# Performance work log

Hardware: AMD Instinct MI355X
Metric: run time of the kernel (lower is better)

## Reference

```python
import jax, jax.numpy as jnp
import numpy as np

B, S, E = 2, 2048, 2048
H, HKV, D = 32, 8, 64  # n_heads, n_kv_heads, head_dim


def _rope(x, cos, sin):
    # x: [B,S,h,D]; cos/sin: [1,S,1,D//2]. Complex rotate on (even,odd) pairs.
    xp = x.reshape(*x.shape[:-1], D // 2, 2)
    x0, x1 = xp[..., 0], xp[..., 1]
    r0 = x0 * cos - x1 * sin
    r1 = x0 * sin + x1 * cos
    return jnp.stack([r0, r1], axis=-1).reshape(x.shape)


def setup_inputs() -> dict:
    key = jax.random.key(0)
    ks = jax.random.split(key, 8)
    sc = 0.02
    # real RoPE frequencies (theta=10000) for realism
    inv = 1.0 / (10000.0 ** (np.arange(0, D, 2, dtype=np.float32) / D))
    t = np.arange(S, dtype=np.float32)
    ang = np.outer(t, inv)  # [S, D/2]
    return {
        "x": jax.random.normal(ks[0], (B, S, E), jnp.float32),
        "start_pos": 0,
        "freqs_cos": jnp.asarray(np.cos(ang))[None, :, None, :],
        "freqs_sin": jnp.asarray(np.sin(ang))[None, :, None, :],
        "wq": jax.random.normal(ks[1], (E, H * D), jnp.float32) * sc,
        "wk": jax.random.normal(ks[2], (E, HKV * D), jnp.float32) * sc,
        "wv": jax.random.normal(ks[3], (E, HKV * D), jnp.float32) * sc,
        "out_w": jax.random.normal(ks[4], (H * D, E), jnp.float32) * sc,
        "out_b": jnp.zeros((E,), jnp.float32),
        "k_cache": jnp.zeros((B, S, HKV, D), jnp.float32),
        "v_cache": jnp.zeros((B, S, HKV, D), jnp.float32),
    }


def reference(x, start_pos, freqs_cos, freqs_sin, wq, wk, wv, out_w, out_b, k_cache, v_cache):
    b, s, _ = x.shape
    q = (x @ wq).reshape(b, s, H, D)
    k = (x @ wk).reshape(b, s, HKV, D)
    v = (x @ wv).reshape(b, s, HKV, D)
    q = _rope(q, freqs_cos[:, :s], freqs_sin[:, :s])
    k = _rope(k, freqs_cos[:, :s], freqs_sin[:, :s])
    # KV-cache append (torch code detaches before writing)
    k_cache = jax.lax.dynamic_update_slice(k_cache, jax.lax.stop_gradient(k), (0, start_pos, 0, 0))
    v_cache = jax.lax.dynamic_update_slice(v_cache, jax.lax.stop_gradient(v), (0, start_pos, 0, 0))
    keys = k_cache[:b, : start_pos + s]    # [b, T, HKV, D]
    values = v_cache[:b, : start_pos + s]
    g = H // HKV
    if g > 1:  # GQA head repeat
        keys = jnp.repeat(keys, g, axis=2)     # [b, T, H, D]
        values = jnp.repeat(values, g, axis=2)
    scores = jnp.einsum("bqhd,bkhd->bhqk", q, keys) / jnp.sqrt(jnp.float32(D))
    att = jax.nn.softmax(scores, axis=-1)  # NOTE: source applies no causal mask
    o = jnp.einsum("bhqk,bkhd->bqhd", att, values).reshape(b, s, H * D)
    return o @ out_w + out_b
```

## Files before the change

### kernel.cpp

```cpp
#include <hip/hip_runtime.h>
#include <math.h>

#define B_    2
#define S_    2048
#define E_    2048
#define H_    32
#define HKV_  8
#define D_    64

typedef __bf16 bf16x8 __attribute__((ext_vector_type(8)));
typedef __bf16 bf16x4 __attribute__((ext_vector_type(4)));
typedef float  f32x4  __attribute__((ext_vector_type(4)));

#define GPTR(x) ((const __attribute__((address_space(1))) void*)(x))
#define LPTR(x) ((__attribute__((address_space(3))) void*)(x))

__global__ __launch_bounds__(256) void convert_kernel(
    const float* __restrict__ in, __bf16* __restrict__ out, int n8)
{
    const int i = blockIdx.x * 256 + threadIdx.x;
    if (i >= n8) return;
    const float4 a = ((const float4*)in)[i * 2];
    const float4 b = ((const float4*)in)[i * 2 + 1];
    bf16x8 o;
    o[0] = (__bf16)a.x; o[1] = (__bf16)a.y; o[2] = (__bf16)a.z; o[3] = (__bf16)a.w;
    o[4] = (__bf16)b.x; o[5] = (__bf16)b.y; o[6] = (__bf16)b.z; o[7] = (__bf16)b.w;
    ((bf16x8*)out)[i] = o;
}

__global__ __launch_bounds__(256) void transpose_convert_kernel(
    const float* __restrict__ in, __bf16* __restrict__ out, int K, int N)
{
    __shared__ float tile[32][33];
    const int k0 = blockIdx.y * 32, n0 = blockIdx.x * 32;
    const int r  = threadIdx.x >> 3;
    const int c4 = (threadIdx.x & 7) * 4;
    const float4 v = *(const float4*)&in[(size_t)(k0 + r) * N + n0 + c4];
    tile[r][c4 + 0] = v.x; tile[r][c4 + 1] = v.y;
    tile[r][c4 + 2] = v.z; tile[r][c4 + 3] = v.w;
    __syncthreads();
    ushort4 o;
    __bf16 h0 = (__bf16)tile[c4 + 0][r]; o.x = __builtin_bit_cast(unsigned short, h0);
    __bf16 h1 = (__bf16)tile[c4 + 1][r]; o.y = __builtin_bit_cast(unsigned short, h1);
    __bf16 h2 = (__bf16)tile[c4 + 2][r]; o.z = __builtin_bit_cast(unsigned short, h2);
    __bf16 h3 = (__bf16)tile[c4 + 3][r]; o.w = __builtin_bit_cast(unsigned short, h3);
    *(ushort4*)&out[(size_t)(n0 + r) * K + k0 + c4] = o;
}

__device__ __forceinline__ void gemm_mfma_body(
    const __bf16* __restrict__ A, const __bf16* __restrict__ Bt,
    int m0, int n0, int K, __bf16* sA, __bf16* sB, f32x4 acc[4][4])
{
    const int t    = threadIdx.x;
    const int w    = t >> 6;
    const int lane = t & 63;
    const int col  = lane & 15;
    const int quad = lane >> 4;
    const int wrow = (w >> 1) * 64;
    const int wcol = (w & 1) * 64;

    const int row0 = t >> 3;
    const int c0   = t & 7;

    for (int k0 = 0; k0 < K; k0 += 64) {
#pragma unroll
        for (int it = 0; it < 4; ++it) {
            const int row  = it * 32 + row0;
            const int csrc = c0 ^ (row & 7);
            __builtin_amdgcn_global_load_lds(
                GPTR(A + (size_t)(m0 + row) * K + k0 + csrc * 8),
                LPTR(sA + (it * 256 + t) * 8), 16, 0, 0);
        }
#pragma unroll
        for (int it = 0; it < 4; ++it) {
            const int row  = it * 32 + row0;
            const int csrc = c0 ^ (row & 7);
            __builtin_amdgcn_global_load_lds(
                GPTR(Bt + (size_t)(n0 + row) * K + k0 + csrc * 8),
                LPTR(sB + (it * 256 + t) * 8), 16, 0, 0);
        }
        __syncthreads();

#pragma unroll
        for (int kk = 0; kk < 2; ++kk) {
            bf16x8 af[4], bfr[4];
#pragma unroll
            for (int i = 0; i < 4; ++i) {
                const int m = wrow + i * 16 + col;
                af[i] = *(const bf16x8*)&sA[m * 64 + (((kk * 4 + quad) ^ (m & 7)) * 8)];
            }
#pragma unroll
            for (int j = 0; j < 4; ++j) {
                const int n = wcol + j * 16 + col;
                bfr[j] = *(const bf16x8*)&sB[n * 64 + (((kk * 4 + quad) ^ (n & 7)) * 8)];
            }
#pragma unroll
            for (int i = 0; i < 4; ++i)
#pragma unroll
                for (int j = 0; j < 4; ++j)
                    acc[i][j] = __builtin_amdgcn_mfma_f32_16x16x32_bf16(
                        af[i], bfr[j], acc[i][j], 0, 0, 0);
        }
        __syncthreads();
    }
}

__global__ __launch_bounds__(256) void gemm_qkv_kernel(
    const __bf16* __restrict__ xb, const __bf16* __restrict__ wT,
    __bf16* __restrict__ qb, __bf16* __restrict__ kb, __bf16* __restrict__ vb)
{
    __shared__ __bf16 sA[128 * 64];
    __shared__ __bf16 sB[128 * 64];
    f32x4 acc[4][4];
#pragma unroll
    for (int i = 0; i < 4; ++i)
#pragma unroll
        for (int j = 0; j < 4; ++j) acc[i][j] = (f32x4){0.f, 0.f, 0.f, 0.f};

    const int bx = blockIdx.x;
    const int m0 = blockIdx.y * 128;
    gemm_mfma_body(xb, wT, m0, bx * 128, E_, sA, sB, acc);

    __bf16* Cp; int ldc, nb;
    if (bx < 16)      { Cp = qb; ldc = H_ * D_;   nb = bx * 128; }
    else if (bx < 20) { Cp = kb; ldc = HKV_ * D_; nb = (bx - 16) * 128; }
    else              { Cp = vb; ldc = HKV_ * D_; nb = (bx - 20) * 128; }

    const int lane = threadIdx.x & 63;
    const int col  = lane & 15;
    const int quad = lane >> 4;
    const int wrow = ((threadIdx.x >> 6) >> 1) * 64;
    const int wcol = ((threadIdx.x >> 6) & 1) * 64;
#pragma unroll
    for (int i = 0; i < 4; ++i)
#pragma unroll
        for (int j = 0; j < 4; ++j)
#pragma unroll
            for (int r = 0; r < 4; ++r) {
                const int m = m0 + wrow + i * 16 + quad * 4 + r;
                const int n = nb + wcol + j * 16 + col;
                Cp[(size_t)m * ldc + n] = (__bf16)acc[i][j][r];
            }
}

__global__ __launch_bounds__(256) void gemm_out_kernel(
    const __bf16* __restrict__ ob, const __bf16* __restrict__ woT,
    const float* __restrict__ bias, float* __restrict__ out)
{
    __shared__ __bf16 sA[128 * 64];
    __shared__ __bf16 sB[128 * 64];
    f32x4 acc[4][4];
#pragma unroll
    for (int i = 0; i < 4; ++i)
#pragma unroll
        for (int j = 0; j < 4; ++j) acc[i][j] = (f32x4){0.f, 0.f, 0.f, 0.f};

    const int m0 = blockIdx.y * 128;
    const int n0 = blockIdx.x * 128;
    gemm_mfma_body(ob, woT, m0, n0, H_ * D_, sA, sB, acc);

    const int lane = threadIdx.x & 63;
    const int col  = lane & 15;
    const int quad = lane >> 4;
    const int wrow = ((threadIdx.x >> 6) >> 1) * 64;
    const int wcol = ((threadIdx.x >> 6) & 1) * 64;
#pragma unroll
    for (int i = 0; i < 4; ++i)
#pragma unroll
        for (int j = 0; j < 4; ++j)
#pragma unroll
            for (int r = 0; r < 4; ++r) {
                const int m = m0 + wrow + i * 16 + quad * 4 + r;
                const int n = n0 + wcol + j * 16 + col;
                out[(size_t)m * E_ + n] = acc[i][j][r] + bias[n];
            }
}

__global__ __launch_bounds__(256) void rope_kernel(
    __bf16* __restrict__ p, const float* __restrict__ fc,
    const float* __restrict__ fs, int nh, int npairs)
{
    const int i = blockIdx.x * 256 + threadIdx.x;
    if (i >= npairs) return;
    const int pair = i & 31;
    const int row  = i >> 5;
    const int s    = (row / nh) % S_;
    const unsigned int v = ((const unsigned int*)p)[i];
    const float x0 = (float)__builtin_bit_cast(__bf16, (unsigned short)(v & 0xffff));
    const float x1 = (float)__builtin_bit_cast(__bf16, (unsigned short)(v >> 16));
    const float c  = fc[s * 32 + pair];
    const float sn = fs[s * 32 + pair];
    const __bf16 r0 = (__bf16)(x0 * c - x1 * sn);
    const __bf16 r1 = (__bf16)(x0 * sn + x1 * c);
    ((unsigned int*)p)[i] =
        ((unsigned int)__builtin_bit_cast(unsigned short, r1) << 16) |
        (unsigned int)__builtin_bit_cast(unsigned short, r0);
}

__global__ __launch_bounds__(256, 2) void attn_kernel(
    const __bf16* __restrict__ qw, const __bf16* __restrict__ kw,
    const __bf16* __restrict__ vw, __bf16* __restrict__ ow)
{
    __shared__ __bf16 sK [64][72];
    __shared__ __bf16 sVT[64][72];
    __shared__ __bf16 sP [4][64][72];

    const int t    = threadIdx.x;
    const int w    = t >> 6;
    const int lane = t & 63;
    const int col  = lane & 15;
    const int quad = lane >> 4;

    const int bh  = blockIdx.y;
    const int b   = bh >> 5;
    const int h   = bh & 31;
    const int kvh = h >> 2;
    const int q0w = blockIdx.x * 256 + w * 64;

    const int KSTR = HKV_ * D_;

    bf16x8 bQ[4][2];
#pragma unroll
    for (int qf = 0; qf < 4; ++qf) {
        const __bf16* qrow = qw + (((size_t)b * S_ + q0w + qf * 16 + col) * H_ + h) * D_;
        bQ[qf][0] = ((const bf16x8*)qrow)[quad];
        bQ[qf][1] = ((const bf16x8*)qrow)[4 + quad];
    }

    f32x4 O[4][4];
#pragma unroll
    for (int qf = 0; qf < 4; ++qf)
#pragma unroll
        for (int dt = 0; dt < 4; ++dt) O[qf][dt] = (f32x4){0.f, 0.f, 0.f, 0.f};
    float lr[4] = {0.f, 0.f, 0.f, 0.f};

    const __bf16* kbase = kw + ((size_t)b * S_ * HKV_ + kvh) * D_;
    const __bf16* vbase = vw + ((size_t)b * S_ * HKV_ + kvh) * D_;

    const int kkey = t >> 2;
    const int kd   = (t & 3) * 16;
    const int vkp  = (t & 31) * 2;
    const int vdg  = (t >> 5) * 4;

    for (int j0 = 0; j0 < S_; j0 += 64) {
        {
            const __bf16* kr = kbase + (size_t)(j0 + kkey) * KSTR + kd;
            *(bf16x8*)&sK[kkey][kd]     = ((const bf16x8*)kr)[0];
            *(bf16x8*)&sK[kkey][kd + 8] = ((const bf16x8*)kr)[1];
        }
#pragma unroll
        for (int r = 0; r < 64; r += 32) {
            const __bf16* v0 = vbase + (size_t)(j0 + vkp) * KSTR + vdg + r;
            const __bf16* v1 = v0 + KSTR;
            const ushort4 ua = *(const ushort4*)v0;
            const ushort4 uc = *(const ushort4*)v1;
            *(unsigned int*)&sVT[vdg + r + 0][vkp] = ((unsigned int)uc.x << 16) | ua.x;
            *(unsigned int*)&sVT[vdg + r + 1][vkp] = ((unsigned int)uc.y << 16) | ua.y;
            *(unsigned int*)&sVT[vdg + r + 2][vkp] = ((unsigned int)uc.z << 16) | ua.z;
            *(unsigned int*)&sVT[vdg + r + 3][vkp] = ((unsigned int)uc.w << 16) | ua.w;
        }
        __syncthreads();

#pragma unroll
        for (int st = 0; st < 4; ++st) {
            const bf16x8 aK0 = *(const bf16x8*)&sK[st * 16 + col][quad * 8];
            const bf16x8 aK1 = *(const bf16x8*)&sK[st * 16 + col][32 + quad * 8];
#pragma unroll
            for (int qf = 0; qf < 4; ++qf) {
                f32x4 sc = (f32x4){0.f, 0.f, 0.f, 0.f};
                sc = __builtin_amdgcn_mfma_f32_16x16x32_bf16(aK0, bQ[qf][0], sc, 0, 0, 0);
                sc = __builtin_amdgcn_mfma_f32_16x16x32_bf16(aK1, bQ[qf][1], sc, 0, 0, 0);
                bf16x4 pk;
                float psum = 0.f;
#pragma unroll
                for (int r = 0; r < 4; ++r) {
                    const float p = __expf(sc[r] * 0.125f);
                    psum += p;
                    pk[r] = (__bf16)p;
                }
                lr[qf] += psum;
                *(bf16x4*)&sP[w][qf * 16 + col][st * 16 + quad * 4] = pk;
            }
        }

        bf16x8 vbf[4][2];
#pragma unroll
        for (int dt = 0; dt < 4; ++dt) {
            vbf[dt][0] = *(const bf16x8*)&sVT[dt * 16 + col][quad * 8];
            vbf[dt][1] = *(const bf16x8*)&sVT[dt * 16 + col][32 + quad * 8];
        }
#pragma unroll
        for (int qf = 0; qf < 4; ++qf) {
            const bf16x8 pa0 = *(const bf16x8*)&sP[w][qf * 16 + col][quad * 8];
            const bf16x8 pa1 = *(const bf16x8*)&sP[w][qf * 16 + col][32 + quad * 8];
#pragma unroll
            for (int dt = 0; dt < 4; ++dt) {
                O[qf][dt] = __builtin_amdgcn_mfma_f32_16x16x32_bf16(pa0, vbf[dt][0], O[qf][dt], 0, 0, 0);
                O[qf][dt] = __builtin_amdgcn_mfma_f32_16x16x32_bf16(pa1, vbf[dt][1], O[qf][dt], 0, 0, 0);
            }
        }
        __syncthreads();
    }

#pragma unroll
    for (int qf = 0; qf < 4; ++qf) {
        lr[qf] += __shfl_xor(lr[qf], 16);
        lr[qf] += __shfl_xor(lr[qf], 32);
    }

#pragma unroll
    for (int qf = 0; qf < 4; ++qf)
#pragma unroll
        for (int r = 0; r < 4; ++r) {
            const float lv  = __shfl(lr[qf], quad * 4 + r);
            const float inv = 1.f / lv;
            const int   qr  = q0w + qf * 16 + quad * 4 + r;
            __bf16* orow = ow + (((size_t)b * S_ + qr) * H_ + h) * D_;
#pragma unroll
            for (int dt = 0; dt < 4; ++dt)
                orow[dt * 16 + col] = (__bf16)(O[qf][dt][r] * inv);
        }
}

extern "C" void kernel_launch(void* const* d_in, const int* in_sizes, int n_in,
                              void* d_out, int out_size, void* d_ws, size_t ws_size,
                              hipStream_t stream)
{
    const float* x  = (const float*)d_in[0];
    const float* fc = (const float*)d_in[2];
    const float* fs = (const float*)d_in[3];
    const float* wq = (const float*)d_in[4];
    const float* wk = (const float*)d_in[5];
    const float* wv = (const float*)d_in[6];
    const float* wo = (const float*)d_in[7];
    const float* obias = (const float*)d_in[8];
    float* out = (float*)d_out;

    __bf16* ws  = (__bf16*)d_ws;
    __bf16* xb  = ws;
    __bf16* wT  = xb  + (size_t)4096 * 2048;
    __bf16* woT = wT  + (size_t)3072 * 2048;
    __bf16* qb  = woT + (size_t)2048 * 2048;
    __bf16* kb  = qb  + (size_t)B_ * S_ * H_ * D_;
    __bf16* vb  = kb  + (size_t)B_ * S_ * HKV_ * D_;
    __bf16* obf = vb  + (size_t)B_ * S_ * HKV_ * D_;

    convert_kernel<<<4096, 256, 0, stream>>>(x, xb, 4096 * 2048 / 8);
    transpose_convert_kernel<<<dim3(64, 64), 256, 0, stream>>>(wq, wT, E_, 2048);
    transpose_convert_kernel<<<dim3(16, 64), 256, 0, stream>>>(wk, wT + (size_t)2048 * 2048, E_, 512);
    transpose_convert_kernel<<<dim3(16, 64), 256, 0, stream>>>(wv, wT + (size_t)2560 * 2048, E_, 512);
    transpose_convert_kernel<<<dim3(64, 64), 256, 0, stream>>>(wo, woT, H_ * D_, E_);

    gemm_qkv_kernel<<<dim3(24, 32), 256, 0, stream>>>(xb, wT, qb, kb, vb);

    rope_kernel<<<(B_ * S_ * H_ * 32 + 255) / 256, 256, 0, stream>>>(
        qb, fc, fs, H_, B_ * S_ * H_ * 32);
    rope_kernel<<<(B_ * S_ * HKV_ * 32 + 255) / 256, 256, 0, stream>>>(
        kb, fc, fs, HKV_, B_ * S_ * HKV_ * 32);

    attn_kernel<<<dim3(S_ / 256, B_ * H_), 256, 0, stream>>>(qb, kb, vb, obf);

    gemm_out_kernel<<<dim3(16, 32), 256, 0, stream>>>(obf, woT, obias, out);
}
```

Baseline: 385.0 us.

## Split PV into two 32-key halves with swizzled smaller P buffer and prescaled Q

Restructures the per-tile softmax/PV stage so that P for 32 keys at a time is written to a smaller shared buffer (64x32 per wave instead of 64x72) using an XOR swizzle to avoid bank conflicts, then consumed immediately by the PV MFMAs. This shrinks LDS footprint (potentially raising occupancy) and interleaves QK and PV work. Q is also prescaled by 1/sqrt(D) at load so the exp skips a multiply, at the cost of extra bf16 rounding of Q.

```diff
diff --git a/kernel.cpp b/kernel.cpp
--- a/kernel.cpp
+++ b/kernel.cpp
@@ -203,13 +203,14 @@
 {
     __shared__ __bf16 sK [64][72];
     __shared__ __bf16 sVT[64][72];
-    __shared__ __bf16 sP [4][64][72];
+    __shared__ __bf16 sP [4][64][32];
 
     const int t    = threadIdx.x;
     const int w    = t >> 6;
     const int lane = t & 63;
     const int col  = lane & 15;
     const int quad = lane >> 4;
+    const int sw   = (col & 7) ^ ((col >> 3) & 1);
 
     const int bh  = blockIdx.y;
     const int b   = bh >> 5;
@@ -223,8 +224,15 @@
 #pragma unroll
     for (int qf = 0; qf < 4; ++qf) {
         const __bf16* qrow = qw + (((size_t)b * S_ + q0w + qf * 16 + col) * H_ + h) * D_;
-        bQ[qf][0] = ((const bf16x8*)qrow)[quad];
-        bQ[qf][1] = ((const bf16x8*)qrow)[4 + quad];
+        bf16x8 r0 = ((const bf16x8*)qrow)[quad];
+        bf16x8 r1 = ((const bf16x8*)qrow)[4 + quad];
+#pragma unroll
+        for (int e = 0; e < 8; ++e) {
+            r0[e] = (__bf16)((float)r0[e] * 0.125f);
+            r1[e] = (__bf16)((float)r1[e] * 0.125f);
+        }
+        bQ[qf][0] = r0;
+        bQ[qf][1] = r1;
     }
 
     f32x4 O[4][4];
@@ -262,41 +270,48 @@
         __syncthreads();
 
 #pragma unroll
-        for (int st = 0; st < 4; ++st) {
-            const bf16x8 aK0 = *(const bf16x8*)&sK[st * 16 + col][quad * 8];
-            const bf16x8 aK1 = *(const bf16x8*)&sK[st * 16 + col][32 + quad * 8];
+        for (int half = 0; half < 2; ++half) {
+#pragma unroll
+            for (int sti = 0; sti < 2; ++sti) {
+                const int st = half * 2 + sti;
+                const bf16x8 aK0 = *(const bf16x8*)&sK[st * 16 + col][quad * 8];
+                const bf16x8 aK1 = *(const bf16x8*)&sK[st * 16 + col][32 + quad * 8];
+#pragma unroll
+                for (int qf = 0; qf < 4; ++qf) {
+                    f32x4 sc = (f32x4){0.f, 0.f, 0.f, 0.f};
+                    sc = __builtin_amdgcn_mfma_f32_16x16x32_bf16(aK0, bQ[qf][0], sc, 0, 0, 0);
+                    sc = __builtin_amdgcn_mfma_f32_16x16x32_bf16(aK1, bQ[qf][1], sc, 0, 0, 0);
+                    bf16x4 pk;
+                    float psum = 0.f;
+#pragma unroll
+                    for (int r = 0; r < 4; ++r) {
+                        const float p = __expf(sc[r]);
+                        psum += p;
+                        pk[r] = (__bf16)p;
+                    }
+                    lr[qf] += psum;
+                    const int gs = (sti * 4 + quad) ^ sw;
+                    *(bf16x4*)&sP[w][qf * 16 + col][gs * 4] = pk;
+                }
+            }
+
+            bf16x8 vbf[4];
+#pragma unroll
+            for (int dt = 0; dt < 4; ++dt)
+                vbf[dt] = *(const bf16x8*)&sVT[dt * 16 + col][half * 32 + quad * 8];
 #pragma unroll
             for (int qf = 0; qf < 4; ++qf) {
-                f32x4 sc = (f32x4){0.f, 0.f, 0.f, 0.f};
-                sc = __builtin_amdgcn_mfma_f32_16x16x32_bf16(aK0, bQ[qf][0], sc, 0, 0, 0);
-                sc = __builtin_amdgcn_mfma_f32_16x16x32_bf16(aK1, bQ[qf][1], sc, 0, 0, 0);
-                bf16x4 pk;
-                float psum = 0.f;
-#pragma unroll
-                for (int r = 0; r < 4; ++r) {
-                    const float p = __expf(sc[r] * 0.125f);
-                    psum += p;
-                    pk[r] = (__bf16)p;
-                }
-                lr[qf] += psum;
-                *(bf16x4*)&sP[w][qf * 16 + col][st * 16 + quad * 4] = pk;
-            }
-        }
-
-        bf16x8 vbf[4][2];
-#pragma unroll
-        for (int dt = 0; dt < 4; ++dt) {
-            vbf[dt][0] = *(const bf16x8*)&sVT[dt * 16 + col][quad * 8];
-            vbf[dt][1] = *(const bf16x8*)&sVT[dt * 16 + col][32 + quad * 8];
-        }
-#pragma unroll
-        for (int qf = 0; qf < 4; ++qf) {
-            const bf16x8 pa0 = *(const bf16x8*)&sP[w][qf * 16 + col][quad * 8];
-            const bf16x8 pa1 = *(const bf16x8*)&sP[w][qf * 16 + col][32 + quad * 8];
-#pragma unroll
-            for (int dt = 0; dt < 4; ++dt) {
-                O[qf][dt] = __builtin_amdgcn_mfma_f32_16x16x32_bf16(pa0, vbf[dt][0], O[qf][dt], 0, 0, 0);
-                O[qf][dt] = __builtin_amdgcn_mfma_f32_16x16x32_bf16(pa1, vbf[dt][1], O[qf][dt], 0, 0, 0);
+                const int gs0 = (2 * quad)     ^ sw;
+                const int gs1 = (2 * quad + 1) ^ sw;
+                const bf16x4 lo = *(const bf16x4*)&sP[w][qf * 16 + col][gs0 * 4];
+                const bf16x4 hi = *(const bf16x4*)&sP[w][qf * 16 + col][gs1 * 4];
+                bf16x8 pa;
+                pa[0] = lo[0]; pa[1] = lo[1]; pa[2] = lo[2]; pa[3] = lo[3];
+                pa[4] = hi[0]; pa[5] = hi[1]; pa[6] = hi[2]; pa[7] = hi[3];
+#pragma unroll
+                for (int dt = 0; dt < 4; ++dt)
+                    O[qf][dt] = __builtin_amdgcn_mfma_f32_16x16x32_bf16(
+                        pa, vbf[dt], O[qf][dt], 0, 0, 0);
             }
         }
         __syncthreads();
```

Result: no change. 390.5 us (+1.4%).
